# Kernel optimization log

Hardware: AMD Instinct MI355X
Metric: run time of the kernel (lower is better)

Reference implementation:

```python
import jax, jax.numpy as jnp
import numpy as np

N_NODES = 50000


def _graphconv(h, W, b, src, dst, norm_src, norm_dst, activation):
    # DGL GraphConv, norm='both': scale by out-degree^{-1/2} on src side,
    # aggregate (copy_u + sum), scale by in-degree^{-1/2} on dst side.
    in_f, out_f = W.shape
    h = h * norm_src[:, None]
    if in_f > out_f:
        # mult W first to reduce message size (matches DGL branch)
        h = h @ W
        h = jax.ops.segment_sum(h[src], dst, num_segments=N_NODES)
    else:
        h = jax.ops.segment_sum(h[src], dst, num_segments=N_NODES)
        h = h @ W
    h = h * norm_dst[:, None] + b
    if activation:
        h = jax.nn.relu(h)
    return h


def setup_inputs() -> dict:
    key = jax.random.key(0)
    ks = jax.random.split(key, 10)
    N, E = N_NODES, 800000
    in_feats, n_hidden, n_classes = 256, 128, 64
    features = jax.random.normal(ks[0], (N, in_feats), dtype=jnp.float32)
    src = jax.random.randint(ks[1], (E,), 0, N, dtype=jnp.int32)
    dst = jax.random.randint(ks[2], (E,), 0, N, dtype=jnp.int32)
    def glorot(k, shape):
        lim = float(np.sqrt(6.0 / (shape[0] + shape[1])))
        return jax.random.uniform(k, shape, jnp.float32, -lim, lim)
    return {
        "features": features,
        "W1": glorot(ks[3], (in_feats, n_hidden)), "b1": jnp.zeros((n_hidden,), jnp.float32),
        "W2": glorot(ks[4], (n_hidden, n_hidden)), "b2": jnp.zeros((n_hidden,), jnp.float32),
        "W3": glorot(ks[5], (n_hidden, n_classes)), "b3": jnp.zeros((n_classes,), jnp.float32),
        "src": src, "dst": dst,
    }


def reference(features, W1, b1, W2, b2, W3, b3, src, dst):
    ones = jnp.ones(src.shape, jnp.float32)
    deg_out = jax.ops.segment_sum(ones, src, num_segments=N_NODES)
    deg_in = jax.ops.segment_sum(ones, dst, num_segments=N_NODES)
    norm_src = jax.lax.rsqrt(jnp.maximum(deg_out, 1.0))
    norm_dst = jax.lax.rsqrt(jnp.maximum(deg_in, 1.0))
    h = features
    # dropout in eval mode (identity) for deterministic baseline
    h = _graphconv(h, W1, b1, src, dst, norm_src, norm_dst, activation=True)
    h = _graphconv(h, W2, b2, src, dst, norm_src, norm_dst, activation=True)
    h = _graphconv(h, W3, b3, src, dst, norm_src, norm_dst, activation=False)
    return h
```

## Files before the change

### kernel.cpp

```cpp
#include <hip/hip_runtime.h>
#include <math.h>


typedef _Float16 half8 __attribute__((ext_vector_type(8)));
typedef float floatx4 __attribute__((ext_vector_type(4)));

#define TILE  1024
#define BCAP  8192
#define PKW   64
#define EPT   4
#define SPLIT 4

__global__ __launch_bounds__(256) void bin_edges(
    const int* __restrict__ src, const int* __restrict__ dst, int E, int NB,
    int* __restrict__ gcurD, int* __restrict__ gcurS,
    ushort2* __restrict__ binD, unsigned short* __restrict__ binS)
{
    __shared__ int lcntD[256], curD[256];
    __shared__ int lcntS[256], curS[256];

    const int tid = threadIdx.x;
    const int tile0 = blockIdx.x * TILE;
    const int tn = min(TILE, E - tile0);

    lcntD[tid] = 0;
    lcntS[tid] = 0;
    __syncthreads();

    unsigned short es[EPT], ed[EPT];
    unsigned char ebD[EPT], ebS[EPT];
    int nl = 0;
    for (int i = tid; i < tn; i += 256) {
        int s = src[tile0 + i], d = dst[tile0 + i];
        es[nl] = (unsigned short)s; ed[nl] = (unsigned short)d;
        ebD[nl] = (unsigned char)(d >> 8);
        ebS[nl] = (unsigned char)(s >> 8);
        nl++;
        atomicAdd(&lcntD[d >> 8], 1);
        atomicAdd(&lcntS[s >> 8], 1);
    }
    __syncthreads();

    if (tid < NB) {
        curD[tid] = (lcntD[tid] > 0) ? atomicAdd(&gcurD[tid], lcntD[tid]) : 0;
        curS[tid] = (lcntS[tid] > 0) ? atomicAdd(&gcurS[tid], lcntS[tid]) : 0;
    }
    __syncthreads();

    for (int j = 0; j < nl; j++) {
        int bD = ebD[j];
        int pD = atomicAdd(&curD[bD], 1);
        if (pD < BCAP) {
            ushort2 u; u.x = es[j]; u.y = ed[j];
            binD[(size_t)bD * BCAP + pD] = u;
        }
        int bS = ebS[j];
        int pS = atomicAdd(&curS[bS], 1);
        if (pS < BCAP) binS[(size_t)bS * BCAP + pS] = es[j];
    }
}

__global__ __launch_bounds__(256) void lists_counts(
    const ushort2* __restrict__ binD, const int* __restrict__ gcurD,
    const unsigned short* __restrict__ binS, const int* __restrict__ gcurS,
    unsigned short* __restrict__ packed, int* __restrict__ cntI,
    int* __restrict__ cntO, int N, unsigned short padv)
{
    __shared__ unsigned short stage[64 * PKW];
    __shared__ int lcnt[64];
    __shared__ int h[64];
    const int tid = threadIdx.x;
    const int b = blockIdx.x / SPLIT;
    const int part = blockIdx.x - b * SPLIT;
    const int nlo = (b << 8) + part * 64;

    if (tid < 64) { lcnt[tid] = 0; h[tid] = 0; }
    {
        unsigned int pp = (unsigned int)padv | ((unsigned int)padv << 16);
        uint4 v; v.x = pp; v.y = pp; v.z = pp; v.w = pp;
        for (int i = tid; i < 64 * PKW / 8; i += 256)
            ((uint4*)stage)[i] = v;
    }
    __syncthreads();

    const int nD = min(gcurD[b], BCAP);
    const ushort2* ebD = binD + (size_t)b * BCAP;
    for (int i = tid; i < nD; i += 256) {
        ushort2 e = ebD[i];
        int ld = (int)e.y - nlo;
        if ((unsigned)ld < 64u) {
            int p = atomicAdd(&lcnt[ld], 1);
            if (p < PKW) stage[ld * PKW + p] = e.x;
        }
    }
    const int nS = min(gcurS[b], BCAP);
    const unsigned short* ebS = binS + (size_t)b * BCAP;
    for (int i = tid; i < nS; i += 256) {
        int ls = (int)ebS[i] - nlo;
        if ((unsigned)ls < 64u) atomicAdd(&h[ls], 1);
    }
    __syncthreads();

    if (tid < 64) {
        int node = nlo + tid;
        if (node < N) {
            cntI[node] = min(lcnt[tid], PKW);
            cntO[node] = h[tid];
        }
    }
    const int wave = tid >> 6, lane = tid & 63;
    for (int ld = wave; ld < 64; ld += 4) {
        int nd = nlo + ld;
        if (nd < N)
            packed[(size_t)nd * PKW + lane] = stage[ld * PKW + lane];
    }
}

__global__ __launch_bounds__(256) void wprep(
    const float* __restrict__ W1, const float* __restrict__ W2,
    const float* __restrict__ W3, _Float16* __restrict__ WT1,
    _Float16* __restrict__ WT2, _Float16* __restrict__ WT3,
    int* __restrict__ gcur, _Float16* __restrict__ z0,
    _Float16* __restrict__ z1)
{
    int i = blockIdx.x * 256 + threadIdx.x;
    if (i < 512) gcur[i] = 0;
    else if (i < 640) z0[i - 512] = (_Float16)0.f;
    else if (i < 768) z1[i - 640] = (_Float16)0.f;
    if (i < 256 * 128) {
        int k = i / 128, n = i - k * 128;
        WT1[(size_t)n * 256 + k] = (_Float16)W1[i];
    } else if (i < 256 * 128 + 128 * 128) {
        int r = i - 256 * 128;
        int k = r / 128, n = r - k * 128;
        WT2[(size_t)n * 128 + k] = (_Float16)W2[r];
    } else if (i < 256 * 128 + 128 * 128 + 128 * 64) {
        int r = i - 256 * 128 - 128 * 128;
        int k = r / 64, n = r - k * 64;
        WT3[(size_t)n * 128 + k] = (_Float16)W3[r];
    }
}

template<int K, int NC, bool A_FP32>
__global__ __launch_bounds__(256) void gemm_mfma(
    const void* __restrict__ A_, const _Float16* __restrict__ WT,
    const int* __restrict__ cnt_rs,
    const int* __restrict__ cnt_nd, const float* __restrict__ bias,
    int do_relu, const int* __restrict__ cnt_ns,
    _Float16* __restrict__ C, int M)
{
    constexpr int NT  = NC / 16;
    constexpr int KC  = 128;
    constexpr int LDW = KC + 8;
    __shared__ _Float16 Bs[NC * LDW];

    const int tid  = threadIdx.x;
    const int wave = tid >> 6;
    const int lane = tid & 63;
    const int quad = lane >> 4;
    const int l16  = lane & 15;

    const int row_base = blockIdx.x * 128 + wave * 32;
    const int ar0 = min(row_base + l16, M - 1);
    const int ar1 = min(row_base + 16 + l16, M - 1);

    floatx4 acc[2][NT];
#pragma unroll
    for (int m = 0; m < 2; m++)
#pragma unroll
        for (int t = 0; t < NT; t++)
            acc[m][t] = (floatx4){0.f, 0.f, 0.f, 0.f};

    float rs0 = 1.0f, rs1 = 1.0f;
    if (A_FP32 && cnt_rs) {
        rs0 = rsqrtf(fmaxf((float)cnt_rs[ar0], 1.0f));
        rs1 = rsqrtf(fmaxf((float)cnt_rs[ar1], 1.0f));
    }

    const float*    Af = (const float*)A_;
    const _Float16* Ah = (const _Float16*)A_;

    for (int kc = 0; kc < K; kc += KC) {
#pragma unroll
        for (int s = tid; s < NC * (KC / 8); s += 256) {
            int row  = s >> 4;
            int col8 = s & 15;
            half8 v = *(const half8*)&WT[(size_t)row * K + kc + col8 * 8];
            *(half8*)&Bs[row * LDW + col8 * 8] = v;
        }
        __syncthreads();
#pragma unroll
        for (int k0 = 0; k0 < KC; k0 += 32) {
            half8 a0, a1;
            if (A_FP32) {
                const float* p0 = &Af[(size_t)ar0 * K + kc + k0 + quad * 8];
                const float* p1 = &Af[(size_t)ar1 * K + kc + k0 + quad * 8];
                float4 f0 = *(const float4*)p0;
                float4 f1 = *(const float4*)(p0 + 4);
                float4 g0 = *(const float4*)p1;
                float4 g1 = *(const float4*)(p1 + 4);
                a0[0] = (_Float16)(f0.x * rs0); a0[1] = (_Float16)(f0.y * rs0);
                a0[2] = (_Float16)(f0.z * rs0); a0[3] = (_Float16)(f0.w * rs0);
                a0[4] = (_Float16)(f1.x * rs0); a0[5] = (_Float16)(f1.y * rs0);
                a0[6] = (_Float16)(f1.z * rs0); a0[7] = (_Float16)(f1.w * rs0);
                a1[0] = (_Float16)(g0.x * rs1); a1[1] = (_Float16)(g0.y * rs1);
                a1[2] = (_Float16)(g0.z * rs1); a1[3] = (_Float16)(g0.w * rs1);
                a1[4] = (_Float16)(g1.x * rs1); a1[5] = (_Float16)(g1.y * rs1);
                a1[6] = (_Float16)(g1.z * rs1); a1[7] = (_Float16)(g1.w * rs1);
            } else {
                a0 = *(const half8*)&Ah[(size_t)ar0 * K + kc + k0 + quad * 8];
                a1 = *(const half8*)&Ah[(size_t)ar1 * K + kc + k0 + quad * 8];
            }
#pragma unroll
            for (int t = 0; t < NT; t++) {
                half8 b = *(const half8*)&Bs[(t * 16 + l16) * LDW + k0 + quad * 8];
                acc[0][t] = __builtin_amdgcn_mfma_f32_16x16x32_f16(a0, b, acc[0][t], 0, 0, 0);
                acc[1][t] = __builtin_amdgcn_mfma_f32_16x16x32_f16(a1, b, acc[1][t], 0, 0, 0);
            }
        }
        __syncthreads();
    }

#pragma unroll
    for (int m = 0; m < 2; m++) {
#pragma unroll
        for (int t = 0; t < NT; t++) {
            int col = t * 16 + l16;
            float bv = bias ? bias[col] : 0.f;
#pragma unroll
            for (int r = 0; r < 4; r++) {
                int row_o = row_base + m * 16 + quad * 4 + r;
                if (row_o < M) {
                    float v = acc[m][t][r];
                    if (cnt_nd) v *= rsqrtf(fmaxf((float)cnt_nd[row_o], 1.0f));
                    v += bv;
                    if (do_relu) v = fmaxf(v, 0.f);
                    if (cnt_ns) v *= rsqrtf(fmaxf((float)cnt_ns[row_o], 1.0f));
                    C[(size_t)row_o * NC + col] = (_Float16)v;
                }
            }
        }
    }
}

__global__ __launch_bounds__(256) void gather128(
    const _Float16* __restrict__ msg, const int* __restrict__ cntI,
    const int* __restrict__ cntO, const unsigned short* __restrict__ packed,
    const float* __restrict__ bias, int do_relu, int use_nd, int use_ns,
    _Float16* __restrict__ out, int N)
{
    int node = (blockIdx.x * 256 + threadIdx.x) >> 6;
    if (node >= N) return;
    int lane = threadIdx.x & 63;
    int grp = lane >> 4, l16 = lane & 15;

    int len = min(cntI[node], PKW);
    const unsigned short* bl = packed + (size_t)node * PKW;
    const half8* mp = (const half8*)msg;

    float a[8];
#pragma unroll
    for (int h = 0; h < 8; h++) a[h] = 0.f;

    int iters = (len + 15) >> 4;
    if (iters < 1) iters = 1;
    for (int it = 0; it < iters; it++) {
        int j = it * 16 + grp;
        int s0 = bl[j], s1 = bl[j + 4], s2 = bl[j + 8], s3 = bl[j + 12];
        half8 v0 = mp[(size_t)s0 * 16 + l16];
        half8 v1 = mp[(size_t)s1 * 16 + l16];
        half8 v2 = mp[(size_t)s2 * 16 + l16];
        half8 v3 = mp[(size_t)s3 * 16 + l16];
#pragma unroll
        for (int h = 0; h < 8; h++)
            a[h] += ((float)v0[h] + (float)v1[h]) + ((float)v2[h] + (float)v3[h]);
    }
#pragma unroll
    for (int h = 0; h < 8; h++) {
        a[h] += __shfl_xor(a[h], 16);
        a[h] += __shfl_xor(a[h], 32);
    }

    if (grp == 0) {
        float sc = use_nd ? rsqrtf(fmaxf((float)len, 1.0f)) : 1.0f;
        float pp = use_ns ? rsqrtf(fmaxf((float)cntO[node], 1.0f)) : 1.0f;
        half8 rv;
#pragma unroll
        for (int h = 0; h < 8; h++) {
            float bv = bias ? bias[l16 * 8 + h] : 0.f;
            float r = a[h] * sc + bv;
            if (do_relu) r = fmaxf(r, 0.f);
            rv[h] = (_Float16)(r * pp);
        }
        ((half8*)out)[(size_t)node * 16 + l16] = rv;
    }
}

__global__ __launch_bounds__(256) void gather64(
    const _Float16* __restrict__ msg, const int* __restrict__ cntI,
    const unsigned short* __restrict__ packed, const float* __restrict__ bias,
    float* __restrict__ out, int N)
{
    int node = (blockIdx.x * 256 + threadIdx.x) >> 6;
    if (node >= N) return;
    int lane = threadIdx.x & 63;
    int grp = lane >> 3, l8 = lane & 7;

    int len = min(cntI[node], PKW);
    const unsigned short* bl = packed + (size_t)node * PKW;
    const half8* mp = (const half8*)msg;

    float a[8];
#pragma unroll
    for (int h = 0; h < 8; h++) a[h] = 0.f;

    int iters = (len + 15) >> 4;
    if (iters < 1) iters = 1;
    for (int it = 0; it < iters; it++) {
        int j = it * 16 + grp;
        int s0 = bl[j], s1 = bl[j + 8];
        half8 v0 = mp[(size_t)s0 * 8 + l8];
        half8 v1 = mp[(size_t)s1 * 8 + l8];
#pragma unroll
        for (int h = 0; h < 8; h++)
            a[h] += (float)v0[h] + (float)v1[h];
    }
#pragma unroll
    for (int h = 0; h < 8; h++) {
        a[h] += __shfl_xor(a[h], 8);
        a[h] += __shfl_xor(a[h], 16);
        a[h] += __shfl_xor(a[h], 32);
    }

    if (grp == 0) {
        float sc = rsqrtf(fmaxf((float)len, 1.0f));
        float4 r0, r1;
        r0.x = a[0] * sc + bias[l8 * 8 + 0];
        r0.y = a[1] * sc + bias[l8 * 8 + 1];
        r0.z = a[2] * sc + bias[l8 * 8 + 2];
        r0.w = a[3] * sc + bias[l8 * 8 + 3];
        r1.x = a[4] * sc + bias[l8 * 8 + 4];
        r1.y = a[5] * sc + bias[l8 * 8 + 5];
        r1.z = a[6] * sc + bias[l8 * 8 + 6];
        r1.w = a[7] * sc + bias[l8 * 8 + 7];
        float4* op = (float4*)&out[(size_t)node * 64 + l8 * 8];
        op[0] = r0;
        op[1] = r1;
    }
}

extern "C" void kernel_launch(void* const* d_in, const int* in_sizes, int n_in,
                              void* d_out, int out_size, void* d_ws, size_t ws_size,
                              hipStream_t stream)
{
    const float* X  = (const float*)d_in[0];
    const float* W1 = (const float*)d_in[1];
    const float* b1 = (const float*)d_in[2];
    const float* W2 = (const float*)d_in[3];
    const float* b2 = (const float*)d_in[4];
    const float* W3 = (const float*)d_in[5];
    const float* b3 = (const float*)d_in[6];
    const int*   src = (const int*)d_in[7];
    const int*   dst = (const int*)d_in[8];

    const int N = in_sizes[0] / 256;
    const int E = in_sizes[7];
    const int NB = (N + 255) >> 8;

    char* base = (char*)d_ws;
    size_t cur = 0;
    auto alloc = [&](size_t bytes) -> void* {
        void* p = base + cur;
        cur += (bytes + 255) & ~(size_t)255;
        return p;
    };
    int* gcur2 = (int*)alloc((size_t)2 * 256 * 4);
    int* gcurD = gcur2;
    int* gcurS = gcur2 + 256;
    ushort2*        binD   = (ushort2*)alloc((size_t)NB * BCAP * 4);
    unsigned short* binS   = (unsigned short*)alloc((size_t)NB * BCAP * 2);
    unsigned short* packed = (unsigned short*)alloc((size_t)N * PKW * 2);
    int* cntO = (int*)alloc((size_t)N * 4);
    int* cntI = (int*)alloc((size_t)N * 4);
    _Float16* Bh0 = (_Float16*)alloc(((size_t)N + 1) * 128 * 2);
    _Float16* Bh1 = (_Float16*)alloc(((size_t)N + 1) * 128 * 2);
    _Float16* WT1 = (_Float16*)alloc((size_t)256 * 128 * 2);
    _Float16* WT2 = (_Float16*)alloc((size_t)128 * 128 * 2);
    _Float16* WT3 = (_Float16*)alloc((size_t)128 * 64 * 2);

    const int tblk = (E + TILE - 1) / TILE;
    const int gblk = (N + 127) / 128;
    const int wblk = (N + 3) / 4;

    wprep<<<(256*128 + 128*128 + 128*64 + 255) / 256, 256, 0, stream>>>(
        W1, W2, W3, WT1, WT2, WT3,
        gcur2, Bh0 + (size_t)N * 128, Bh1 + (size_t)N * 128);
    bin_edges<<<tblk, 256, 0, stream>>>(src, dst, E, NB, gcurD, gcurS, binD, binS);
    lists_counts<<<NB * SPLIT, 256, 0, stream>>>(binD, gcurD, binS, gcurS,
                                                 packed, cntI, cntO, N,
                                                 (unsigned short)N);

    gemm_mfma<256, 128, true><<<gblk, 256, 0, stream>>>(
        X, WT1, cntO, nullptr, nullptr, 0, nullptr, Bh0, N);
    gather128<<<wblk, 256, 0, stream>>>(
        Bh0, cntI, cntO, packed, b1, 1, 1, 1, Bh1, N);

    gather128<<<wblk, 256, 0, stream>>>(
        Bh1, cntI, cntO, packed, nullptr, 0, 0, 0, Bh0, N);
    gemm_mfma<128, 128, false><<<gblk, 256, 0, stream>>>(
        Bh0, WT2, nullptr, cntI, b2, 1, cntO, Bh1, N);

    gemm_mfma<128, 64, false><<<(N + 1 + 127) / 128, 256, 0, stream>>>(
        Bh1, WT3, nullptr, nullptr, nullptr, 0, nullptr, Bh0, N + 1);
    gather64<<<wblk, 256, 0, stream>>>(
        Bh0, cntI, packed, b3, (float*)d_out, N);
}
```

Baseline: 297.5 us.

## Fuse layer-2 gather, layer-2 GEMM and layer-3 GEMM into one kernel

Replaces three launches (layer-2 gather, layer-2 GEMM, layer-3 GEMM) with one kernel. Each 512-thread block gathers 128 destination rows into LDS, runs the 128x128 MFMA GEMM with bias, ReLU and degree norms, then runs the 128x64 GEMM from LDS and writes the layer-3 messages. This removes the global round-trips of two intermediate 50000x128 fp16 tensors and two launches. In exchange, each wave serializes the gather over 16 rows and the block holds about 70KB of LDS, which limits occupancy during the latency-bound gather. It also writes the zero padding row at index N itself.

```diff
diff --git a/kernel.cpp b/kernel.cpp
--- a/kernel.cpp
+++ b/kernel.cpp
@@ -243,6 +243,144 @@
     }
 }
 
+__global__ __launch_bounds__(512) void layer23(
+    const _Float16* __restrict__ H1s, const int* __restrict__ cntI,
+    const int* __restrict__ cntO, const unsigned short* __restrict__ packed,
+    const _Float16* __restrict__ WT2, const _Float16* __restrict__ WT3,
+    const float* __restrict__ b2, _Float16* __restrict__ M3, int N)
+{
+    constexpr int LDW = 136;
+    __shared__ _Float16 agg[128 * LDW];
+    __shared__ _Float16 Bs[128 * LDW];
+
+    const int tid  = threadIdx.x;
+    const int w    = tid >> 6;
+    const int lane = tid & 63;
+    const int quad = lane >> 4;
+    const int l16  = lane & 15;
+    const int grp  = lane >> 4;
+    const int base = blockIdx.x * 128;
+
+    if (blockIdx.x == 0 && tid < 8) {
+        half8 zv;
+#pragma unroll
+        for (int h = 0; h < 8; h++) zv[h] = (_Float16)0.f;
+        ((half8*)(M3 + (size_t)N * 64))[tid] = zv;
+    }
+
+    const half8* mp = (const half8*)H1s;
+    for (int i = 0; i < 16; i++) {
+        const int row  = w * 16 + i;
+        const int node = base + row;
+        float a[8];
+#pragma unroll
+        for (int h = 0; h < 8; h++) a[h] = 0.f;
+        if (node < N) {
+            int len = cntI[node];
+            const unsigned short* bl = packed + (size_t)node * PKW;
+            int iters = (len + 15) >> 4;
+            if (iters < 1) iters = 1;
+            for (int it = 0; it < iters; it++) {
+                int j = it * 16 + grp;
+                int s0 = bl[j], s1 = bl[j + 4], s2 = bl[j + 8], s3 = bl[j + 12];
+                half8 v0 = mp[(size_t)s0 * 16 + l16];
+                half8 v1 = mp[(size_t)s1 * 16 + l16];
+                half8 v2 = mp[(size_t)s2 * 16 + l16];
+                half8 v3 = mp[(size_t)s3 * 16 + l16];
+#pragma unroll
+                for (int h = 0; h < 8; h++)
+                    a[h] += ((float)v0[h] + (float)v1[h]) + ((float)v2[h] + (float)v3[h]);
+            }
+#pragma unroll
+            for (int h = 0; h < 8; h++) {
+                a[h] += __shfl_xor(a[h], 16);
+                a[h] += __shfl_xor(a[h], 32);
+            }
+        }
+        if (grp == 0) {
+            half8 rv;
+#pragma unroll
+            for (int h = 0; h < 8; h++) rv[h] = (_Float16)a[h];
+            *(half8*)&agg[row * LDW + l16 * 8] = rv;
+        }
+    }
+    __syncthreads();
+
+#pragma unroll
+    for (int s = tid; s < 128 * 16; s += 512) {
+        int row = s >> 4, col8 = s & 15;
+        *(half8*)&Bs[row * LDW + col8 * 8] =
+            *(const half8*)&WT2[(size_t)row * 128 + col8 * 8];
+    }
+    __syncthreads();
+
+    floatx4 acc[8];
+#pragma unroll
+    for (int t = 0; t < 8; t++) acc[t] = (floatx4){0.f, 0.f, 0.f, 0.f};
+#pragma unroll
+    for (int k0 = 0; k0 < 128; k0 += 32) {
+        half8 a0 = *(const half8*)&agg[(w * 16 + l16) * LDW + k0 + quad * 8];
+#pragma unroll
+        for (int t = 0; t < 8; t++) {
+            half8 b = *(const half8*)&Bs[(t * 16 + l16) * LDW + k0 + quad * 8];
+            acc[t] = __builtin_amdgcn_mfma_f32_16x16x32_f16(a0, b, acc[t], 0, 0, 0);
+        }
+    }
+    float rsI_[4], rsO_[4];
+#pragma unroll
+    for (int r = 0; r < 4; r++) {
+        int row_o = base + w * 16 + quad * 4 + r;
+        int ro = min(row_o, N - 1);
+        rsI_[r] = rsqrtf(fmaxf((float)cntI[ro], 1.0f));
+        rsO_[r] = rsqrtf(fmaxf((float)cntO[ro], 1.0f));
+    }
+#pragma unroll
+    for (int t = 0; t < 8; t++) {
+        int col = t * 16 + l16;
+        float bv = b2[col];
+#pragma unroll
+        for (int r = 0; r < 4; r++) {
+            int row_l = w * 16 + quad * 4 + r;
+            float v = acc[t][r] * rsI_[r] + bv;
+            v = fmaxf(v, 0.f);
+            v *= rsO_[r];
+            agg[row_l * LDW + col] = (_Float16)v;
+        }
+    }
+    __syncthreads();
+
+#pragma unroll
+    for (int s = tid; s < 64 * 16; s += 512) {
+        int row = s >> 4, col8 = s & 15;
+        *(half8*)&Bs[row * LDW + col8 * 8] =
+            *(const half8*)&WT3[(size_t)row * 128 + col8 * 8];
+    }
+    __syncthreads();
+
+    floatx4 acc3[4];
+#pragma unroll
+    for (int t = 0; t < 4; t++) acc3[t] = (floatx4){0.f, 0.f, 0.f, 0.f};
+#pragma unroll
+    for (int k0 = 0; k0 < 128; k0 += 32) {
+        half8 a0 = *(const half8*)&agg[(w * 16 + l16) * LDW + k0 + quad * 8];
+#pragma unroll
+        for (int t = 0; t < 4; t++) {
+            half8 b = *(const half8*)&Bs[(t * 16 + l16) * LDW + k0 + quad * 8];
+            acc3[t] = __builtin_amdgcn_mfma_f32_16x16x32_f16(a0, b, acc3[t], 0, 0, 0);
+        }
+    }
+#pragma unroll
+    for (int t = 0; t < 4; t++) {
+        int col = t * 16 + l16;
+#pragma unroll
+        for (int r = 0; r < 4; r++) {
+            int row_o = base + w * 16 + quad * 4 + r;
+            if (row_o < N)
+                M3[(size_t)row_o * 64 + col] = (_Float16)acc3[t][r];
+        }
+    }
+}
+
 __global__ __launch_bounds__(256) void gather128(
     const _Float16* __restrict__ msg, const int* __restrict__ cntI,
     const int* __restrict__ cntO, const unsigned short* __restrict__ packed,
@@ -405,13 +543,9 @@
     gather128<<<wblk, 256, 0, stream>>>(
         Bh0, cntI, cntO, packed, b1, 1, 1, 1, Bh1, N);
 
-    gather128<<<wblk, 256, 0, stream>>>(
-        Bh1, cntI, cntO, packed, nullptr, 0, 0, 0, Bh0, N);
-    gemm_mfma<128, 128, false><<<gblk, 256, 0, stream>>>(
-        Bh0, WT2, nullptr, cntI, b2, 1, cntO, Bh1, N);
-
-    gemm_mfma<128, 64, false><<<(N + 1 + 127) / 128, 256, 0, stream>>>(
-        Bh1, WT3, nullptr, nullptr, nullptr, 0, nullptr, Bh0, N + 1);
+    layer23<<<gblk, 512, 0, stream>>>(
+        Bh1, cntI, cntO, packed, WT2, WT3, b2, Bh0, N);
+
     gather64<<<wblk, 256, 0, stream>>>(
         Bh0, cntI, packed, b3, (float*)d_out, N);
 }
```

New measurement: 269.0 us. -9.6%, faster.
